# Kernel optimization log

Hardware: AMD Instinct MI355X
Metric: run time of the kernel (lower is better)

The kernel has to match this reference:

```python
import jax, jax.numpy as jnp
import numpy as np

V, E, H, L = 100000, 128, 512, 9
B, T = 64, 512


def setup_inputs() -> dict:
    key = jax.random.key(0)
    ks = jax.random.split(key, 8)
    text = jax.random.randint(ks[0], (B, T), 0, V, dtype=jnp.int32)
    labels = jax.random.randint(ks[1], (B, T), 0, L, dtype=jnp.int32)
    embed = jax.random.normal(ks[2], (V, E), jnp.float32) * 0.02
    Wx = jax.random.normal(ks[3], (E, 4 * H), jnp.float32) * (1.0 / np.sqrt(E))
    Wh = jax.random.normal(ks[4], (H, 4 * H), jnp.float32) * (1.0 / np.sqrt(H))
    # Keras LSTM default: zero bias with unit forget-gate bias (gate order i,f,c,o)
    b = jnp.zeros((4 * H,), jnp.float32).at[H:2 * H].set(1.0)
    Wd = jax.random.normal(ks[5], (H, L), jnp.float32) * (1.0 / np.sqrt(H))
    bd = jnp.zeros((L,), jnp.float32)
    trans = jax.random.uniform(ks[6], (L, L), jnp.float32)
    return dict(text=text, labels=labels, embed=embed, Wx=Wx, Wh=Wh, b=b,
                Wd=Wd, bd=bd, trans=trans)


def _lstm(x, Wx, Wh, b):
    # x: [B,T,E] -> h: [B,T,H]; Keras gate order i,f,c,o
    Bx, Tx, _ = x.shape
    Hh = Wh.shape[0]
    xg = jnp.einsum('bte,eg->btg', x, Wx) + b  # precompute input projections [B,T,4H]

    def step(carry, g_t):
        h, c = carry
        g = g_t + h @ Wh
        i, f, cg, o = jnp.split(g, 4, axis=-1)
        c = jax.nn.sigmoid(f) * c + jax.nn.sigmoid(i) * jnp.tanh(cg)
        h = jax.nn.sigmoid(o) * jnp.tanh(c)
        return (h, c), h

    init = (jnp.zeros((Bx, Hh), x.dtype), jnp.zeros((Bx, Hh), x.dtype))
    _, hs = jax.lax.scan(step, init, jnp.moveaxis(xg, 1, 0))
    return jnp.moveaxis(hs, 0, 1)


def _crf_log_likelihood(logits, labels, lens, trans):
    # tfa.text.crf_log_likelihood: score(seq) - log_norm (forward algorithm)
    Bl, Tl, Ll = logits.shape
    t_idx = jnp.arange(Tl)
    mask = t_idx[None, :] < lens[:, None]  # [B,T]
    unary = jnp.take_along_axis(logits, labels[..., None], axis=2)[..., 0]
    unary = jnp.where(mask, unary, 0.0).sum(-1)
    binary = trans[labels[:, :-1], labels[:, 1:]]
    bmask = t_idx[1:][None, :] < lens[:, None]  # transition t->t+1 counts iff t+1 < len
    binary = jnp.where(bmask, binary, 0.0).sum(-1)
    score = unary + binary

    def step(alpha, xs):
        lg, t = xs  # lg: [B,L]
        new = jax.scipy.special.logsumexp(alpha[:, :, None] + trans[None], axis=1) + lg
        alpha = jnp.where((t < lens)[:, None], new, alpha)
        return alpha, None

    alpha0 = logits[:, 0]
    xs = (jnp.moveaxis(logits[:, 1:], 1, 0), jnp.arange(1, Tl))
    alpha, _ = jax.lax.scan(step, alpha0, xs)
    log_norm = jax.scipy.special.logsumexp(alpha, axis=-1)
    return score - log_norm


def reference(text, labels, embed, Wx, Wh, b, Wd, bd, trans):
    lens = jnp.sum((text != 0).astype(jnp.int32), axis=-1)
    x = embed[text]                      # [B,T,E] (dropout inactive at inference)
    h = _lstm(x, Wx, Wh, b)              # [B,T,H]
    logits = h @ Wd + bd                 # [B,T,L]
    ll = _crf_log_likelihood(logits, labels, lens, trans)  # [B]
    return logits, lens, ll
```

## Files before the change

### kernel.cpp

```cpp
#include <hip/hip_runtime.h>
#include <hip/hip_bf16.h>

#define V_SZ 100000
#define E_SZ 128
#define H_SZ 512
#define L_SZ 9
#define B_SZ 64
#define T_SZ 512
#define G4   (4*H_SZ)

#define LOGITS_N (B_SZ*T_SZ*L_SZ)
#define HS_BYTES ((size_t)B_SZ*T_SZ*H_SZ*2)
#define SENT32 0x7FC07FC0u
#define SENT64 0x7FC07FC07FC07FC0ull

typedef short bf16x8 __attribute__((ext_vector_type(8)));
typedef float f32x4  __attribute__((ext_vector_type(4)));

static __device__ __forceinline__ unsigned short f2bf(float x){
  unsigned int u = __builtin_bit_cast(unsigned int, x);
  unsigned int r = (u + 0x7fffu + ((u >> 16) & 1u)) >> 16;
  return (unsigned short)r;
}
static __device__ __forceinline__ float bf2f(unsigned short b){
  unsigned int u = ((unsigned int)b) << 16;
  return __builtin_bit_cast(float, u);
}
static __device__ __forceinline__ float sig_f(float x){
  return 1.f / (1.f + __expf(-x));
}
static __device__ __forceinline__ float tanh_f(float x){
  float a = fabsf(x);
  float e = __expf(-2.f * a);
  float t = (1.f - e) / (1.f + e);
  return copysignf(t, x);
}

__global__ void k_reset(unsigned long long* __restrict__ hs64){
  const long n = HS_BYTES / 8;
  for (long i = (long)blockIdx.x*256 + threadIdx.x; i < n; i += (long)gridDim.x*256)
    __hip_atomic_store(&hs64[i], SENT64, __ATOMIC_RELAXED, __HIP_MEMORY_SCOPE_AGENT);
}

__global__ void k_lens(const int* __restrict__ text, float* __restrict__ out_lens){
  int b = blockIdx.x;
  int c = 0;
  for (int t = threadIdx.x; t < T_SZ; t += 256)
    c += (text[b*T_SZ + t] != 0);
  for (int off = 32; off; off >>= 1) c += __shfl_down(c, off, 64);
  __shared__ int sred[4];
  int w = threadIdx.x >> 6;
  if ((threadIdx.x & 63) == 0) sred[w] = c;
  __syncthreads();
  if (threadIdx.x == 0)
    out_lens[b] = (float)(sred[0] + sred[1] + sred[2] + sred[3]);
}

__global__ __launch_bounds__(256, 1)
void k_lstm(const int* __restrict__ text, const float* __restrict__ embed,
            const float* __restrict__ Wx, const float* __restrict__ Wh,
            const float* __restrict__ bias, unsigned short* __restrict__ hs)
{
  const int g    = blockIdx.x & 7;
  const int j    = blockIdx.x >> 3;
  const int n0   = j * 16;
  const int tid  = threadIdx.x;
  const int w    = tid >> 6;
  const int lane = tid & 63;
  const int q    = lane >> 4;
  const int l16  = lane & 15;
  const int gate = l16 & 3;
  const int cq   = l16 >> 2;

  __shared__ unsigned short h_lds[2][16*512];
  __shared__ unsigned short x_lds[2][16*128];
  __shared__ int text_lds[8*T_SZ];

  for (int i = tid; i < 2*16*512; i += 256) ((unsigned short*)h_lds)[i] = 0;
  for (int i = tid; i < 2*16*128; i += 256) ((unsigned short*)x_lds)[i] = 0;
  for (int i = tid; i < 8*T_SZ;   i += 256)
    text_lds[i] = text[(g*8 + (i >> 9))*T_SZ + (i & 511)];

  const int hcol = n0 + w*4 + cq;
  const int gcol = gate*H_SZ + hcol;
  bf16x8 Whf[16];
#pragma unroll
  for (int kk = 0; kk < 16; ++kk){
    bf16x8 v;
#pragma unroll
    for (int jj = 0; jj < 8; ++jj)
      v[jj] = (short)f2bf(Wh[(long)(kk*32 + q*8 + jj)*G4 + gcol]);
    Whf[kk] = v;
  }
  bf16x8 Wxf[4];
#pragma unroll
  for (int kk = 0; kk < 4; ++kk){
    bf16x8 v;
#pragma unroll
    for (int jj = 0; jj < 8; ++jj)
      v[jj] = (short)f2bf(Wx[(long)(kk*32 + q*8 + jj)*G4 + gcol]);
    Wxf[kk] = v;
  }
  const float biasv = bias[gcol];

  float cs[4] = {0.f, 0.f, 0.f, 0.f};
  const bool isPub = (gate == 0) && (cq == 0) && (q < 2);

  unsigned short* ppub[4];
#pragma unroll
  for (int rg = 0; rg < 4; ++rg)
    ppub[rg] = hs + ((long)(g*8 + q*4 + rg)*T_SZ)*H_SZ + n0 + w*4;

  const int xr = tid >> 5;
  const int c4 = (tid & 31) * 4;
  const int cb = c4 * 2;
  unsigned short* xdst[2];
#pragma unroll
  for (int pb = 0; pb < 2; ++pb)
    xdst[pb] = (unsigned short*)((char*)x_lds[pb] + xr*256 + (cb ^ (xr << 4)));

  __syncthreads();

  {
    int tok = text_lds[xr*T_SZ + 0];
    const float4 xv = *(const float4*)(embed + (long)tok*E_SZ + c4);
    unsigned short* pp = xdst[0];
    pp[0] = f2bf(xv.x); pp[1] = f2bf(xv.y); pp[2] = f2bf(xv.z); pp[3] = f2bf(xv.w);
  }

  for (int t = 0; t < T_SZ; ++t){
    const int par = t & 1;

    if (t > 0){
      unsigned long long v[4];
      int it = 0; bool ok;
      do {
        ok = true;
#pragma unroll
        for (int c = 0; c < 4; ++c){
          int chunk = tid + 256*c;
          int hr    = chunk >> 7;
          int k4    = chunk & 127;
          v[c] = __hip_atomic_load(
              (const unsigned long long*)(hs + ((long)(g*8 + hr)*T_SZ + (t-1))*H_SZ + k4*4),
              __ATOMIC_RELAXED, __HIP_MEMORY_SCOPE_AGENT);
        }
#pragma unroll
        for (int c = 0; c < 4; ++c){
          unsigned int lo = (unsigned int)v[c], hi = (unsigned int)(v[c] >> 32);
          ok = ok && (lo != SENT32) && (hi != SENT32);
        }
      } while (!ok && ++it < (1 << 20));
#pragma unroll
      for (int c = 0; c < 4; ++c){
        int chunk = tid + 256*c;
        int hr    = chunk >> 7;
        int k4    = chunk & 127;
        *(unsigned long long*)((char*)h_lds[par] + hr*1024 + ((k4*8) ^ (hr << 4))) = v[c];
      }
    }
    __syncthreads();

    float4 xv; bool havex = (t + 1 < T_SZ);
    if (havex){
      int tok = text_lds[xr*T_SZ + t + 1];
      xv = *(const float4*)(embed + (long)tok*E_SZ + c4);
    }

    f32x4 acc0 = {biasv, biasv, biasv, biasv};
    f32x4 acc1 = {0.f, 0.f, 0.f, 0.f};
#pragma unroll
    for (int kk = 0; kk < 4; ++kk){
      bf16x8 a = *(const bf16x8*)((const char*)x_lds[par] + l16*256 + ((kk*64 + q*16) ^ (l16 << 4)));
      if (kk & 1) acc1 = __builtin_amdgcn_mfma_f32_16x16x32_bf16(a, Wxf[kk], acc1, 0, 0, 0);
      else        acc0 = __builtin_amdgcn_mfma_f32_16x16x32_bf16(a, Wxf[kk], acc0, 0, 0, 0);
    }
    if (t > 0){
#pragma unroll
      for (int kk = 0; kk < 16; ++kk){
        bf16x8 a = *(const bf16x8*)((const char*)h_lds[par] + l16*1024 + ((kk*64 + q*16) ^ (l16 << 4)));
        if (kk & 1) acc1 = __builtin_amdgcn_mfma_f32_16x16x32_bf16(a, Whf[kk], acc1, 0, 0, 0);
        else        acc0 = __builtin_amdgcn_mfma_f32_16x16x32_bf16(a, Whf[kk], acc0, 0, 0, 0);
      }
    }

#pragma unroll
    for (int rg = 0; rg < 4; ++rg){
      float v  = acc0[rg] + acc1[rg];
      float x1 = __shfl_xor(v, 1, 64);
      float x2 = __shfl_xor(v, 2, 64);
      float x3 = __shfl_xor(v, 3, 64);
      float gi = (gate==0)? v : (gate==1)? x1 : (gate==2)? x2 : x3;
      float gf = (gate==1)? v : (gate==0)? x1 : (gate==3)? x2 : x3;
      float gc = (gate==2)? v : (gate==3)? x1 : (gate==0)? x2 : x3;
      float go = (gate==3)? v : (gate==2)? x1 : (gate==1)? x2 : x3;
      cs[rg] = sig_f(gf)*cs[rg] + sig_f(gi)*tanh_f(gc);
      float hv = sig_f(go)*tanh_f(cs[rg]);
      unsigned int hb = (unsigned int)f2bf(hv);
      unsigned int pr  = (unsigned int)__shfl_xor((int)hb, 4, 64);
      unsigned int pk  = hb | (pr << 16);
      unsigned int pk2 = (unsigned int)__shfl_xor((int)pk, 8, 64);
      unsigned long long p8 = (unsigned long long)pk
                            | ((unsigned long long)pk2 << 32);
      if (isPub)
        __hip_atomic_store((unsigned long long*)ppub[rg], p8,
                           __ATOMIC_RELAXED, __HIP_MEMORY_SCOPE_AGENT);
    }
#pragma unroll
    for (int rg = 0; rg < 4; ++rg) ppub[rg] += H_SZ;

    if (havex){
      unsigned short* pp = xdst[par ^ 1];
      pp[0] = f2bf(xv.x); pp[1] = f2bf(xv.y); pp[2] = f2bf(xv.z); pp[3] = f2bf(xv.w);
    }
  }
}

__global__ void k_logits(const unsigned short* __restrict__ hs,
                         const float* __restrict__ Wd, const float* __restrict__ bd,
                         float* __restrict__ out)
{
  __shared__ float wd_s[H_SZ*L_SZ];
  __shared__ float bd_s[L_SZ];
  for (int i = threadIdx.x; i < H_SZ*L_SZ; i += 128) wd_s[i] = Wd[i];
  if (threadIdx.x < L_SZ) bd_s[threadIdx.x] = bd[threadIdx.x];
  __syncthreads();

  long row = (long)blockIdx.x*128 + threadIdx.x;
  const unsigned short* hp = hs + row*H_SZ;
  float acc[9];
#pragma unroll
  for (int jj = 0; jj < 9; ++jj) acc[jj] = 0.f;
  for (int k = 0; k < H_SZ; k += 8){
    uint4 v = *(const uint4*)(hp + k);
    const unsigned short* u = (const unsigned short*)&v;
#pragma unroll
    for (int l = 0; l < 8; ++l){
      float hf = bf2f(u[l]);
#pragma unroll
      for (int jj = 0; jj < 9; ++jj)
        acc[jj] = fmaf(hf, wd_s[(k + l)*L_SZ + jj], acc[jj]);
    }
  }
  float* op = out + row*L_SZ;
#pragma unroll
  for (int jj = 0; jj < 9; ++jj) op[jj] = acc[jj] + bd_s[jj];
}

__global__ void k_crf(const float* __restrict__ logits, const int* __restrict__ labels,
                      const float* __restrict__ trans, const float* __restrict__ lensf,
                      float* __restrict__ out_ll)
{
  int b = blockIdx.x;
  int lane = threadIdx.x;
  int len = (int)lensf[b];
  const float* lg  = logits + (long)b*T_SZ*L_SZ;
  const int*   lab = labels + b*T_SZ;

  float s = 0.f;
  for (int t = lane; t < T_SZ; t += 64){
    if (t < len){
      s += lg[t*L_SZ + lab[t]];
      if (t >= 1) s += trans[lab[t-1]*L_SZ + lab[t]];
    }
  }
  for (int off = 32; off; off >>= 1) s += __shfl_down(s, off, 64);

  float tr[9];
#pragma unroll
  for (int i = 0; i < 9; ++i) tr[i] = (lane < 9) ? trans[i*L_SZ + lane] : 0.f;
  float alpha = (lane < 9) ? lg[lane] : -1e30f;

  for (int t = 1; t < T_SZ; ++t){
    float tmp[9];
#pragma unroll
    for (int i = 0; i < 9; ++i){
      float ai = __shfl(alpha, i, 64);
      tmp[i] = ai + tr[i];
    }
    float m0 = fmaxf(fmaxf(tmp[0], tmp[1]), tmp[2]);
    float m1 = fmaxf(fmaxf(tmp[3], tmp[4]), tmp[5]);
    float m2 = fmaxf(fmaxf(tmp[6], tmp[7]), tmp[8]);
    float m  = fmaxf(fmaxf(m0, m1), m2);
    float e = 0.f;
#pragma unroll
    for (int i = 0; i < 9; ++i) e += __expf(tmp[i] - m);
    float lgv = (lane < 9) ? lg[t*L_SZ + lane] : 0.f;
    float nv = m + __logf(e) + lgv;
    if (t < len && lane < 9) alpha = nv;
  }

  float mm = (lane < 9) ? alpha : -1e30f;
  for (int off = 8; off; off >>= 1) mm = fmaxf(mm, __shfl_down(mm, off, 64));
  mm = __shfl(mm, 0, 64);
  float ee = (lane < 9) ? __expf(alpha - mm) : 0.f;
  for (int off = 8; off; off >>= 1) ee += __shfl_down(ee, off, 64);
  if (lane == 0) out_ll[b] = s - (mm + __logf(ee));
}

extern "C" void kernel_launch(void* const* d_in, const int* in_sizes, int n_in,
                              void* d_out, int out_size, void* d_ws, size_t ws_size,
                              hipStream_t stream)
{
  const int*   text   = (const int*)  d_in[0];
  const int*   labels = (const int*)  d_in[1];
  const float* embed  = (const float*)d_in[2];
  const float* Wx     = (const float*)d_in[3];
  const float* Wh     = (const float*)d_in[4];
  const float* bias   = (const float*)d_in[5];
  const float* Wd     = (const float*)d_in[6];
  const float* bd     = (const float*)d_in[7];
  const float* trans  = (const float*)d_in[8];

  float* out        = (float*)d_out;
  float* out_logits = out;
  float* out_lens   = out + LOGITS_N;
  float* out_ll     = out + LOGITS_N + B_SZ;

  unsigned short* hs = (unsigned short*)d_ws;

  k_reset <<<2048, 256, 0, stream>>>((unsigned long long*)hs);
  k_lens  <<<B_SZ, 256, 0, stream>>>(text, out_lens);
  k_lstm  <<<256, 256, 0, stream>>>(text, embed, Wx, Wh, bias, hs);
  k_logits<<<256, 128, 0, stream>>>(hs, Wd, bd, out_logits);
  k_crf   <<<B_SZ, 64, 0, stream>>>(out_logits, labels, trans, out_lens, out_ll);
}
```

Before: 1.551 ms.

## Pack 16 batch rows per LSTM block to fill MFMA tiles, halving block count

The recurrent LSTM kernel now gives each block 16 batch rows instead of 8, so the 16-row MFMA tiles carry real data in every row rather than half padding. The grid shrinks from 256 to 128 blocks. Each block now polls and loads twice as much of the previous hidden state per step, and the sentinel check reads only the low half of each word. Token ids are read straight from global memory instead of being staged in LDS, and the LDS zero-initialisation is dropped. The intent is to cut redundant MFMA work and the number of blocks taking part in the per-step cross-block handoff, at the cost of more bytes read per block each step.

```diff
diff --git a/kernel.cpp b/kernel.cpp
--- a/kernel.cpp
+++ b/kernel.cpp
@@ -61,8 +61,8 @@
             const float* __restrict__ Wx, const float* __restrict__ Wh,
             const float* __restrict__ bias, unsigned short* __restrict__ hs)
 {
-  const int g    = blockIdx.x & 7;
-  const int j    = blockIdx.x >> 3;
+  const int p    = blockIdx.x & 3;
+  const int j    = blockIdx.x >> 2;
   const int n0   = j * 16;
   const int tid  = threadIdx.x;
   const int w    = tid >> 6;
@@ -74,12 +74,6 @@
 
   __shared__ unsigned short h_lds[2][16*512];
   __shared__ unsigned short x_lds[2][16*128];
-  __shared__ int text_lds[8*T_SZ];
-
-  for (int i = tid; i < 2*16*512; i += 256) ((unsigned short*)h_lds)[i] = 0;
-  for (int i = tid; i < 2*16*128; i += 256) ((unsigned short*)x_lds)[i] = 0;
-  for (int i = tid; i < 8*T_SZ;   i += 256)
-    text_lds[i] = text[(g*8 + (i >> 9))*T_SZ + (i & 511)];
 
   const int hcol = n0 + w*4 + cq;
   const int gcol = gate*H_SZ + hcol;
@@ -104,55 +98,54 @@
   const float biasv = bias[gcol];
 
   float cs[4] = {0.f, 0.f, 0.f, 0.f};
-  const bool isPub = (gate == 0) && (cq == 0) && (q < 2);
+  const bool isPub = (l16 == 0);
 
   unsigned short* ppub[4];
 #pragma unroll
   for (int rg = 0; rg < 4; ++rg)
-    ppub[rg] = hs + ((long)(g*8 + q*4 + rg)*T_SZ)*H_SZ + n0 + w*4;
-
-  const int xr = tid >> 5;
-  const int c4 = (tid & 31) * 4;
-  const int cb = c4 * 2;
+    ppub[rg] = hs + ((long)(p*16 + q*4 + rg)*T_SZ)*H_SZ + n0 + w*4;
+
+  const int xr = tid >> 4;
+  const int c8 = (tid & 15) * 8;
+  const int cb = c8 * 2;
   unsigned short* xdst[2];
 #pragma unroll
   for (int pb = 0; pb < 2; ++pb)
     xdst[pb] = (unsigned short*)((char*)x_lds[pb] + xr*256 + (cb ^ (xr << 4)));
-
-  __syncthreads();
+  const int* tokp = text + (p*16 + xr)*T_SZ;
 
   {
-    int tok = text_lds[xr*T_SZ + 0];
-    const float4 xv = *(const float4*)(embed + (long)tok*E_SZ + c4);
+    int tok = tokp[0];
+    const float4 xv0 = *(const float4*)(embed + (long)tok*E_SZ + c8);
+    const float4 xv1 = *(const float4*)(embed + (long)tok*E_SZ + c8 + 4);
     unsigned short* pp = xdst[0];
-    pp[0] = f2bf(xv.x); pp[1] = f2bf(xv.y); pp[2] = f2bf(xv.z); pp[3] = f2bf(xv.w);
+    pp[0] = f2bf(xv0.x); pp[1] = f2bf(xv0.y); pp[2] = f2bf(xv0.z); pp[3] = f2bf(xv0.w);
+    pp[4] = f2bf(xv1.x); pp[5] = f2bf(xv1.y); pp[6] = f2bf(xv1.z); pp[7] = f2bf(xv1.w);
   }
 
   for (int t = 0; t < T_SZ; ++t){
     const int par = t & 1;
 
     if (t > 0){
-      unsigned long long v[4];
+      unsigned long long v[8];
       int it = 0; bool ok;
       do {
         ok = true;
 #pragma unroll
-        for (int c = 0; c < 4; ++c){
+        for (int c = 0; c < 8; ++c){
           int chunk = tid + 256*c;
           int hr    = chunk >> 7;
           int k4    = chunk & 127;
           v[c] = __hip_atomic_load(
-              (const unsigned long long*)(hs + ((long)(g*8 + hr)*T_SZ + (t-1))*H_SZ + k4*4),
+              (const unsigned long long*)(hs + ((long)(p*16 + hr)*T_SZ + (t-1))*H_SZ + k4*4),
               __ATOMIC_RELAXED, __HIP_MEMORY_SCOPE_AGENT);
         }
 #pragma unroll
-        for (int c = 0; c < 4; ++c){
-          unsigned int lo = (unsigned int)v[c], hi = (unsigned int)(v[c] >> 32);
-          ok = ok && (lo != SENT32) && (hi != SENT32);
-        }
+        for (int c = 0; c < 8; ++c)
+          ok = ok && ((unsigned int)v[c] != SENT32);
       } while (!ok && ++it < (1 << 20));
 #pragma unroll
-      for (int c = 0; c < 4; ++c){
+      for (int c = 0; c < 8; ++c){
         int chunk = tid + 256*c;
         int hr    = chunk >> 7;
         int k4    = chunk & 127;
@@ -161,10 +154,11 @@
     }
     __syncthreads();
 
-    float4 xv; bool havex = (t + 1 < T_SZ);
+    float4 xv0, xv1; bool havex = (t + 1 < T_SZ);
     if (havex){
-      int tok = text_lds[xr*T_SZ + t + 1];
-      xv = *(const float4*)(embed + (long)tok*E_SZ + c4);
+      int tok = tokp[t + 1];
+      xv0 = *(const float4*)(embed + (long)tok*E_SZ + c8);
+      xv1 = *(const float4*)(embed + (long)tok*E_SZ + c8 + 4);
     }
 
     f32x4 acc0 = {biasv, biasv, biasv, biasv};
@@ -211,7 +205,8 @@
 
     if (havex){
       unsigned short* pp = xdst[par ^ 1];
-      pp[0] = f2bf(xv.x); pp[1] = f2bf(xv.y); pp[2] = f2bf(xv.z); pp[3] = f2bf(xv.w);
+      pp[0] = f2bf(xv0.x); pp[1] = f2bf(xv0.y); pp[2] = f2bf(xv0.z); pp[3] = f2bf(xv0.w);
+      pp[4] = f2bf(xv1.x); pp[5] = f2bf(xv1.y); pp[6] = f2bf(xv1.z); pp[7] = f2bf(xv1.w);
     }
   }
 }
@@ -321,7 +316,7 @@
 
   k_reset <<<2048, 256, 0, stream>>>((unsigned long long*)hs);
   k_lens  <<<B_SZ, 256, 0, stream>>>(text, out_lens);
-  k_lstm  <<<256, 256, 0, stream>>>(text, embed, Wx, Wh, bias, hs);
+  k_lstm  <<<128, 256, 0, stream>>>(text, embed, Wx, Wh, bias, hs);
   k_logits<<<256, 128, 0, stream>>>(hs, Wd, bd, out_logits);
   k_crf   <<<B_SZ, 64, 0, stream>>>(out_logits, labels, trans, out_lens, out_ll);
 }
```

Result: slower. 1.676 ms (+8.1%).
